# Kernel optimization log

Hardware: AMD Instinct MI355X
Metric: run time of the kernel (lower is better)

Reference implementation:

```python
import jax, jax.numpy as jnp
import numpy as np

D_MODEL = 256; D_FC = 1024; N_LEVELS = 4; N_HEADS = 8; N_POINTS = 4
D_HEAD = D_MODEL // N_HEADS
SPATIAL = np.array([[100, 100], [50, 50], [25, 25], [13, 13]], dtype=np.int64)
S_TOTAL = int((SPATIAL[:, 0] * SPATIAL[:, 1]).sum())  # 13294
BATCH = 2


def setup_inputs() -> dict:
    key = jax.random.key(0)
    ks = jax.random.split(key, 16)

    def lin(k, fi, fo):
        s = 1.0 / np.sqrt(fi)
        kw, kb = jax.random.split(k)
        W = jax.random.uniform(kw, (fi, fo), jnp.float32, -s, s)
        b = jax.random.uniform(kb, (fo,), jnp.float32, -s, s)
        return W, b

    W_off, b_off = lin(ks[0], D_MODEL, N_HEADS * N_LEVELS * N_POINTS * 2)
    W_attn, b_attn = lin(ks[1], D_MODEL, N_HEADS * N_LEVELS * N_POINTS)
    W_val, b_val = lin(ks[2], D_MODEL, D_MODEL)
    W_out, b_out = lin(ks[3], D_MODEL, D_MODEL)
    W1, b1 = lin(ks[4], D_MODEL, D_FC)
    W2, b2 = lin(ks[5], D_FC, D_MODEL)
    src = jax.random.normal(ks[6], (BATCH, S_TOTAL, D_MODEL), jnp.float32)
    pos = jax.random.normal(ks[7], (BATCH, S_TOTAL, D_MODEL), jnp.float32)
    reference_points = jax.random.uniform(ks[8], (BATCH, S_TOTAL, N_LEVELS, 2), jnp.float32)
    level_start_index = np.concatenate([[0], np.cumsum(SPATIAL[:, 0] * SPATIAL[:, 1])[:-1]]).astype(np.int64)
    return dict(src=src, pos=pos, reference_points=reference_points,
                spatial_shapes=SPATIAL, level_start_index=level_start_index,
                W_off=W_off, b_off=b_off, W_attn=W_attn, b_attn=b_attn,
                W_val=W_val, b_val=b_val, W_out=W_out, b_out=b_out,
                ln1_g=jnp.ones(D_MODEL, jnp.float32), ln1_b=jnp.zeros(D_MODEL, jnp.float32),
                W1=W1, b1=b1, W2=W2, b2=b2,
                ln2_g=jnp.ones(D_MODEL, jnp.float32), ln2_b=jnp.zeros(D_MODEL, jnp.float32))


def layernorm(x, g, b, eps=1e-5):
    mu = x.mean(-1, keepdims=True)
    var = ((x - mu) ** 2).mean(-1, keepdims=True)
    return (x - mu) * jax.lax.rsqrt(var + eps) * g + b


def ms_deform_attn(query, value_in, ref_pts, shapes,
                   W_off, b_off, W_attn, b_attn, W_val, b_val, W_out, b_out):
    N, Lq, _ = query.shape
    value = (value_in @ W_val + b_val).reshape(N, -1, N_HEADS, D_HEAD)
    off = (query @ W_off + b_off).reshape(N, Lq, N_HEADS, N_LEVELS, N_POINTS, 2)
    attn = (query @ W_attn + b_attn).reshape(N, Lq, N_HEADS, N_LEVELS * N_POINTS)
    attn = jax.nn.softmax(attn, -1).reshape(N, Lq, N_HEADS, N_LEVELS, N_POINTS)
    # offset normalizer is (W_l, H_l) per level
    norm = jnp.array([[w, h] for (h, w) in shapes], dtype=query.dtype)
    loc = ref_pts[:, :, None, :, None, :] + off / norm[None, None, None, :, None, :]
    out = jnp.zeros((N, Lq, N_HEADS, D_HEAD), query.dtype)
    start = 0
    for l, (H_, W_) in enumerate(shapes):
        v = value[:, start:start + H_ * W_].transpose(0, 2, 1, 3)  # [N, heads, HW, d]
        start += H_ * W_
        loc_l = loc[:, :, :, l]  # [N, Lq, heads, P, 2]
        # grid_sample(align_corners=False, padding_mode='zeros'): pixel = loc*size - 0.5
        px = loc_l[..., 0] * W_ - 0.5
        py = loc_l[..., 1] * H_ - 0.5
        x0 = jnp.floor(px); y0 = jnp.floor(py)
        wx = (px - x0)[..., None]; wy = (py - y0)[..., None]
        x0i = x0.astype(jnp.int32); y0i = y0.astype(jnp.int32)

        def samp(xi, yi):
            valid = (xi >= 0) & (xi < W_) & (yi >= 0) & (yi < H_)
            idx = jnp.clip(yi, 0, H_ - 1) * W_ + jnp.clip(xi, 0, W_ - 1)  # [N,Lq,heads,P]
            idx = idx.transpose(0, 2, 1, 3).reshape(N, N_HEADS, Lq * N_POINTS, 1)
            g = jnp.take_along_axis(v, idx, axis=2)  # [N,heads,Lq*P,d]
            g = g.reshape(N, N_HEADS, Lq, N_POINTS, D_HEAD).transpose(0, 2, 1, 3, 4)
            return g * valid[..., None]

        val = (samp(x0i, y0i) * (1 - wx) * (1 - wy)
               + samp(x0i + 1, y0i) * wx * (1 - wy)
               + samp(x0i, y0i + 1) * (1 - wx) * wy
               + samp(x0i + 1, y0i + 1) * wx * wy)  # [N,Lq,heads,P,d]
        out = out + (val * attn[:, :, :, l, :, None]).sum(3)
    return out.reshape(N, Lq, D_MODEL) @ W_out + b_out


def reference(src, pos, reference_points, spatial_shapes, level_start_index,
              W_off, b_off, W_attn, b_attn, W_val, b_val, W_out, b_out,
              ln1_g, ln1_b, W1, b1, W2, b2, ln2_g, ln2_b):
    shapes = [(int(spatial_shapes[l, 0]), int(spatial_shapes[l, 1])) for l in range(N_LEVELS)]
    q = src + pos
    attn_out = ms_deform_attn(q, src, reference_points, shapes,
                              W_off, b_off, W_attn, b_attn, W_val, b_val, W_out, b_out)
    x = layernorm(src + attn_out, ln1_g, ln1_b)  # dropout is identity in eval
    ffn = jax.nn.relu(x @ W1 + b1) @ W2 + b2
    return layernorm(x + ffn, ln2_g, ln2_b)
```

## Files before the change

kernel.cpp:

```cpp
#include <hip/hip_runtime.h>
#include <hip/hip_bf16.h>

#define DM 256
#define STOT 13294
#define MTOT (2 * STOT)

using bf16 = __hip_bfloat16;
typedef __attribute__((ext_vector_type(8))) short short8;
typedef __attribute__((ext_vector_type(4))) float floatx4;

#define GLDS16(g, l) __builtin_amdgcn_global_load_lds( \
    (const __attribute__((address_space(1))) void*)(g), \
    (__attribute__((address_space(3))) void*)(l), 16, 0, 0)

__device__ __forceinline__ float bu2f(unsigned u) { return __uint_as_float(u << 16); }
__device__ __forceinline__ float ldf(const float* p, size_t i) { return p[i]; }
__device__ __forceinline__ float ldf(const bf16* p, size_t i) { return __bfloat162float(p[i]); }
__device__ __forceinline__ void stf(float* p, size_t i, float v) { p[i] = v; }
__device__ __forceinline__ void stf(bf16* p, size_t i, float v) { p[i] = __float2bfloat16(v); }
__device__ __forceinline__ unsigned short f2bu(float f) {
    union { bf16 h; unsigned short u; } c; c.h = __float2bfloat16(f); return c.u;
}

__global__ void detect_dtype(const unsigned* g1, int* flag) {
    if (threadIdx.x == 0 && blockIdx.x == 0)
        *flag = (g1[0] == 0x3F800000u) ? 1 : 0;
}

struct PW { const void* W[6]; const void* B[6]; };

__global__ void prep_weights(PW a, bf16* __restrict__ WT, float* __restrict__ bf,
                             const int* __restrict__ flag) {
    const long id = (long)blockIdx.x * 256 + threadIdx.x;
    const bool f32in = (*flag != 0);
    const int sz[6]  = {65536, 65536, 32768, 65536, 262144, 262144};
    const int Ns[6]  = {256, 256, 128, 256, 1024, 256};
    const int Ksh[6] = {8, 8, 8, 8, 8, 10};
    if (id < 753664) {
        long e = id; int j = 0;
        while (e >= sz[j]) { e -= sz[j]; ++j; }
        const int n = (int)(e >> Ksh[j]);
        const int k = (int)(e & ((1 << Ksh[j]) - 1));
        const size_t src = (size_t)k * Ns[j] + n;
        float v = f32in ? ((const float*)a.W[j])[src] : __bfloat162float(((const bf16*)a.W[j])[src]);
        WT[id] = __float2bfloat16(v);
    } else if (id < 753664 + 2176) {
        long e = id - 753664; int j = 0;
        const int bsz[6] = {256, 256, 128, 256, 1024, 256};
        while (e >= bsz[j]) { e -= bsz[j]; ++j; }
        float v = f32in ? ((const float*)a.B[j])[e] : __bfloat162float(((const bf16*)a.B[j])[e]);
        bf[id - 753664] = v;
    }
}

__global__ void prep_act(const void* __restrict__ src, const void* __restrict__ pos,
                         bf16* __restrict__ sbf, bf16* __restrict__ qbf,
                         const int* __restrict__ flag) {
    const long i = ((long)blockIdx.x * 256 + threadIdx.x) * 8;
    if (i >= (long)MTOT * DM) return;
    unsigned short ps[8], pq[8];
    if (*flag) {
        const float* s = (const float*)src + i;
        const float* p = (const float*)pos + i;
        float4 a0 = *(const float4*)s, a1 = *(const float4*)(s + 4);
        float4 b0 = *(const float4*)p, b1 = *(const float4*)(p + 4);
        const float av[8] = {a0.x, a0.y, a0.z, a0.w, a1.x, a1.y, a1.z, a1.w};
        const float bv[8] = {b0.x, b0.y, b0.z, b0.w, b1.x, b1.y, b1.z, b1.w};
#pragma unroll
        for (int j = 0; j < 8; ++j) { ps[j] = f2bu(av[j]); pq[j] = f2bu(av[j] + bv[j]); }
    } else {
        const unsigned short* s = (const unsigned short*)src + i;
        const unsigned short* p = (const unsigned short*)pos + i;
        uint4 a = *(const uint4*)s, b = *(const uint4*)p;
        const unsigned* ua = (const unsigned*)&a;
        const unsigned* ub = (const unsigned*)&b;
#pragma unroll
        for (int j = 0; j < 4; ++j) {
            float a0 = bu2f(ua[j] & 0xffffu), a1 = bu2f(ua[j] >> 16);
            float b0 = bu2f(ub[j] & 0xffffu), b1 = bu2f(ub[j] >> 16);
            ps[j * 2] = f2bu(a0); ps[j * 2 + 1] = f2bu(a1);
            pq[j * 2] = f2bu(a0 + b0); pq[j * 2 + 1] = f2bu(a1 + b1);
        }
    }
    *(uint4*)((unsigned short*)sbf + i) = *(const uint4*)ps;
    *(uint4*)((unsigned short*)qbf + i) = *(const uint4*)pq;
}

template<bool RELU>
__global__ __launch_bounds__(256, 4)
void gemm_bf16(const bf16* __restrict__ A0, const bf16* __restrict__ A1, int n_a0,
               const bf16* __restrict__ WT, const float* __restrict__ bias,
               bf16* __restrict__ C0, bf16* __restrict__ C1, bf16* __restrict__ C2,
               int M, int N, int K, int ldc0) {
    __shared__ __align__(16) bf16 sh[16384];
    const int t = threadIdx.x;
    const int wave = t >> 6, lane = t & 63;
    const int bm = blockIdx.y * 128, bn = blockIdx.x * 128;
    const bf16* __restrict__ A = (bn < n_a0) ? A0 : A1;
    const int wm = (wave >> 1) * 64, wn = (wave & 1) * 64;
    const int l15 = lane & 15, quad = lane >> 4;
    const int srow = lane >> 2, sko = (lane & 3) * 8;

    floatx4 acc[4][4];
#pragma unroll
    for (int i = 0; i < 4; ++i)
#pragma unroll
        for (int j = 0; j < 4; ++j) acc[i][j] = (floatx4)0.f;

    const int nb = K >> 5;
#pragma unroll
    for (int rh = 0; rh < 2; ++rh) {
        const int rbase = rh * 64 + wave * 16;
        const int gm = min(bm + rbase + srow, M - 1);
        GLDS16(A + (size_t)gm * K + sko, &sh[rbase * 32]);
        GLDS16(WT + (size_t)(bn + rbase + srow) * K + sko, &sh[8192 + rbase * 32]);
    }
    for (int i = 0; i < nb; ++i) {
        __syncthreads();
        if (i + 1 < nb) {
            const int k0 = (i + 1) << 5;
            const int bo = ((i + 1) & 1) * 4096;
#pragma unroll
            for (int rh = 0; rh < 2; ++rh) {
                const int rbase = rh * 64 + wave * 16;
                const int gm = min(bm + rbase + srow, M - 1);
                GLDS16(A + (size_t)gm * K + k0 + sko, &sh[bo + rbase * 32]);
                GLDS16(WT + (size_t)(bn + rbase + srow) * K + k0 + sko, &sh[8192 + bo + rbase * 32]);
            }
        }
        const int bo = (i & 1) * 4096;
        short8 af[4], bfr[4];
#pragma unroll
        for (int mi = 0; mi < 4; ++mi)
            af[mi] = *(const short8*)&sh[bo + (wm + mi * 16 + l15) * 32 + quad * 8];
#pragma unroll
        for (int nj = 0; nj < 4; ++nj)
            bfr[nj] = *(const short8*)&sh[8192 + bo + (wn + nj * 16 + l15) * 32 + quad * 8];
#pragma unroll
        for (int mi = 0; mi < 4; ++mi)
#pragma unroll
            for (int nj = 0; nj < 4; ++nj)
                acc[mi][nj] = __builtin_amdgcn_mfma_f32_16x16x32_bf16(bfr[nj], af[mi], acc[mi][nj], 0, 0, 0);
    }

    bf16* C = C0; int coloff = bn, ldc = ldc0;
    if (C1 != nullptr && bn >= 256) {
        if (C2 != nullptr && bn >= 512) { C = C2; coloff = bn - 512; ldc = 128; }
        else                            { C = C1; coloff = bn - 256; ldc = 256; }
    }
    float4 bv4[4];
#pragma unroll
    for (int nj = 0; nj < 4; ++nj)
        bv4[nj] = *(const float4*)&bias[bn + wn + nj * 16 + quad * 4];
#pragma unroll
    for (int mi = 0; mi < 4; ++mi) {
        const int gm = bm + wm + mi * 16 + l15;
        if (gm >= M) continue;
#pragma unroll
        for (int nj = 0; nj < 4; ++nj) {
            const float bb[4] = {bv4[nj].x, bv4[nj].y, bv4[nj].z, bv4[nj].w};
            unsigned short pk[4];
#pragma unroll
            for (int r = 0; r < 4; ++r) {
                float v = acc[mi][nj][r] + bb[r];
                if (RELU) v = fmaxf(v, 0.f);
                pk[r] = f2bu(v);
            }
            *(uint2*)&C[(size_t)gm * ldc + coloff + wn + nj * 16 + quad * 4] = *(const uint2*)pk;
        }
    }
}

__global__ void softmax16(bf16* __restrict__ a, int total) {
    const int i = blockIdx.x * 256 + threadIdx.x;
    if (i >= total) return;
    unsigned short* p = (unsigned short*)(a + (size_t)i * 16);
    uint4 r0 = *(const uint4*)p, r1 = *(const uint4*)(p + 8);
    float w[16];
    const unsigned* u0 = (const unsigned*)&r0;
    const unsigned* u1 = (const unsigned*)&r1;
#pragma unroll
    for (int j = 0; j < 4; ++j) {
        w[j * 2] = bu2f(u0[j] & 0xffffu); w[j * 2 + 1] = bu2f(u0[j] >> 16);
        w[8 + j * 2] = bu2f(u1[j] & 0xffffu); w[8 + j * 2 + 1] = bu2f(u1[j] >> 16);
    }
    float mx = -1e30f;
#pragma unroll
    for (int j = 0; j < 16; ++j) mx = fmaxf(mx, w[j]);
    float s = 0.f;
#pragma unroll
    for (int j = 0; j < 16; ++j) { w[j] = __expf(w[j] - mx); s += w[j]; }
    const float inv = 1.f / s;
    unsigned short pk[16];
#pragma unroll
    for (int j = 0; j < 16; ++j) pk[j] = f2bu(w[j] * inv);
    *(uint4*)p = *(const uint4*)pk;
    *(uint4*)(p + 8) = *(const uint4*)(pk + 8);
}

__device__ __forceinline__ void corner(const bf16* __restrict__ base, int xi, int yi,
                                       int W_, int H_, float wgt, float* acc) {
    const bool valid = (xi >= 0) & (xi < W_) & (yi >= 0) & (yi < H_);
    const int xc = min(max(xi, 0), W_ - 1);
    const int yc = min(max(yi, 0), H_ - 1);
    const ushort4 v = *(const ushort4*)(base + (size_t)(yc * W_ + xc) * DM);
    const float m = valid ? wgt : 0.f;
    acc[0] += m * bu2f(v.x); acc[1] += m * bu2f(v.y);
    acc[2] += m * bu2f(v.z); acc[3] += m * bu2f(v.w);
}

__global__ void deform_sample(const bf16* __restrict__ value, const bf16* __restrict__ off,
                              const bf16* __restrict__ attw, const void* __restrict__ refp,
                              bf16* __restrict__ out, const int* __restrict__ flag) {
    const int t = threadIdx.x;
    const int q = blockIdx.x * 4 + (t >> 6);
    const int ln = t & 63;
    const int h = ln >> 3, dg = ln & 7;
    const int b = (q >= STOT) ? 1 : 0;

    float w[16];
    {
        const unsigned short* wp = (const unsigned short*)(attw + (size_t)q * 128 + h * 16);
        uint4 r0 = *(const uint4*)wp, r1 = *(const uint4*)(wp + 8);
        const unsigned* u0 = (const unsigned*)&r0;
        const unsigned* u1 = (const unsigned*)&r1;
#pragma unroll
        for (int j = 0; j < 4; ++j) {
            w[j * 2] = bu2f(u0[j] & 0xffffu); w[j * 2 + 1] = bu2f(u0[j] >> 16);
            w[8 + j * 2] = bu2f(u1[j] & 0xffffu); w[8 + j * 2 + 1] = bu2f(u1[j] >> 16);
        }
    }
    float of[32];
    {
        const unsigned short* op = (const unsigned short*)(off + (size_t)q * 256 + h * 32);
#pragma unroll
        for (int c = 0; c < 4; ++c) {
            uint4 r = *(const uint4*)(op + c * 8);
            const unsigned* u = (const unsigned*)&r;
#pragma unroll
            for (int j = 0; j < 4; ++j) {
                of[c * 8 + j * 2] = bu2f(u[j] & 0xffffu);
                of[c * 8 + j * 2 + 1] = bu2f(u[j] >> 16);
            }
        }
    }
    float rxy[8];
    if (*flag) {
        const float* rp = (const float*)refp + (size_t)q * 8;
        float4 r0 = *(const float4*)rp, r1 = *(const float4*)(rp + 4);
        rxy[0] = r0.x; rxy[1] = r0.y; rxy[2] = r0.z; rxy[3] = r0.w;
        rxy[4] = r1.x; rxy[5] = r1.y; rxy[6] = r1.z; rxy[7] = r1.w;
    } else {
        const unsigned short* rp = (const unsigned short*)refp + (size_t)q * 8;
        uint4 r = *(const uint4*)rp;
        const unsigned* u = (const unsigned*)&r;
#pragma unroll
        for (int j = 0; j < 4; ++j) {
            rxy[j * 2] = bu2f(u[j] & 0xffffu); rxy[j * 2 + 1] = bu2f(u[j] >> 16);
        }
    }

    const int Hs[4] = {100, 50, 25, 13};
    const int Ls[4] = {0, 10000, 12500, 13125};
    const bf16* vb = value + (size_t)(b * STOT) * DM + h * 32 + dg * 4;

    float acc[4] = {0.f, 0.f, 0.f, 0.f};
#pragma unroll
    for (int l = 0; l < 4; ++l) {
        const int W_ = Hs[l], H_ = Hs[l];
        const bf16* base = vb + (size_t)Ls[l] * DM;
        const float fw = (float)W_, fh = (float)H_;
#pragma unroll
        for (int p = 0; p < 4; ++p) {
            const float px = rxy[l * 2] * fw + of[(l * 4 + p) * 2] - 0.5f;
            const float py = rxy[l * 2 + 1] * fh + of[(l * 4 + p) * 2 + 1] - 0.5f;
            const float x0f = floorf(px), y0f = floorf(py);
            const float wx = px - x0f, wy = py - y0f;
            const int x0 = (int)x0f, y0 = (int)y0f;
            const float aw = w[l * 4 + p];
            const float ex = 1.f - wx, ey = 1.f - wy;
            corner(base, x0, y0, W_, H_, ex * ey * aw, acc);
            corner(base, x0 + 1, y0, W_, H_, wx * ey * aw, acc);
            corner(base, x0, y0 + 1, W_, H_, ex * wy * aw, acc);
            corner(base, x0 + 1, y0 + 1, W_, H_, wx * wy * aw, acc);
        }
    }
    unsigned short pk[4] = {f2bu(acc[0]), f2bu(acc[1]), f2bu(acc[2]), f2bu(acc[3])};
    *(ushort4*)((unsigned short*)out + (size_t)q * 256 + h * 32 + dg * 4) = *(const ushort4*)pk;
}

template<typename TA, typename TB, typename TW, typename TO>
__device__ __forceinline__ void add_ln_body(const TA* __restrict__ A, const TB* __restrict__ Bv,
                                            const TW* __restrict__ g, const TW* __restrict__ be,
                                            TO* __restrict__ out, float* red) {
    const int r = blockIdx.x;
    const int t = threadIdx.x;
    const size_t idx = (size_t)r * DM + t;
    float v = ldf(A, idx) + ldf(Bv, idx);
    float s = v;
#pragma unroll
    for (int o = 32; o > 0; o >>= 1) s += __shfl_down(s, o, 64);
    const int wave = t >> 6, lane = t & 63;
    if (lane == 0) red[wave] = s;
    __syncthreads();
    const float mean = (red[0] + red[1] + red[2] + red[3]) * (1.f / 256.f);
    const float c = v - mean;
    float s2 = c * c;
#pragma unroll
    for (int o = 32; o > 0; o >>= 1) s2 += __shfl_down(s2, o, 64);
    if (lane == 0) red[4 + wave] = s2;
    __syncthreads();
    const float var = (red[4] + red[5] + red[6] + red[7]) * (1.f / 256.f);
    const float y = c * rsqrtf(var + 1e-5f) * ldf(g, (size_t)t) + ldf(be, (size_t)t);
    stf(out, idx, y);
}

__global__ void add_ln1(const bf16* A, const bf16* Bv, const void* g, const void* be,
                        bf16* out, const int* flag) {
    __shared__ float red[8];
    if (*flag) add_ln_body<bf16, bf16, float, bf16>(A, Bv, (const float*)g, (const float*)be, out, red);
    else       add_ln_body<bf16, bf16, bf16, bf16>(A, Bv, (const bf16*)g, (const bf16*)be, out, red);
}

__global__ void add_ln2(const bf16* A, const bf16* Bv, const void* g, const void* be,
                        void* out, const int* flag) {
    __shared__ float red[8];
    if (*flag) add_ln_body<bf16, bf16, float, float>(A, Bv, (const float*)g, (const float*)be, (float*)out, red);
    else       add_ln_body<bf16, bf16, bf16, bf16>(A, Bv, (const bf16*)g, (const bf16*)be, (bf16*)out, red);
}

extern "C" void kernel_launch(void* const* d_in, const int* in_sizes, int n_in,
                              void* d_out, int out_size, void* d_ws, size_t ws_size,
                              hipStream_t stream) {
    const void* src   = d_in[0];
    const void* pos   = d_in[1];
    const void* refp  = d_in[2];
    const void* W_off = d_in[5];
    const void* b_off = d_in[6];
    const void* W_att = d_in[7];
    const void* b_att = d_in[8];
    const void* W_val = d_in[9];
    const void* b_val = d_in[10];
    const void* W_out = d_in[11];
    const void* b_out = d_in[12];
    const void* ln1g  = d_in[13];
    const void* ln1b  = d_in[14];
    const void* W1    = d_in[15];
    const void* b1    = d_in[16];
    const void* W2    = d_in[17];
    const void* b2    = d_in[18];
    const void* ln2g  = d_in[19];
    const void* ln2b  = d_in[20];

    const size_t M = MTOT;
    bf16* src_bf = (bf16*)d_ws;
    bf16* q_bf   = src_bf + M * 256;
    bf16* v_val  = src_bf + M * 512;
    bf16* v_off  = src_bf + M * 768;
    bf16* v_attn = src_bf + M * 1024;
    bf16* v_samp = src_bf + M * 1152;
    bf16* v_tmp  = src_bf + M * 1408;
    bf16* v_x    = q_bf;
    bf16* v_h    = v_val;
    bf16* Y      = src_bf;
    bf16* WT     = src_bf + M * 1664;
    float* biasf = (float*)(WT + 753664);
    int* flag    = (int*)(biasf + 2176);

    dim3 blk(256);
    const int mg = (MTOT + 127) / 128;

    detect_dtype<<<1, 64, 0, stream>>>((const unsigned*)ln1g, flag);

    PW pw;
    pw.W[0] = W_val; pw.W[1] = W_off; pw.W[2] = W_att; pw.W[3] = W_out; pw.W[4] = W1; pw.W[5] = W2;
    pw.B[0] = b_val; pw.B[1] = b_off; pw.B[2] = b_att; pw.B[3] = b_out; pw.B[4] = b1; pw.B[5] = b2;
    prep_weights<<<(753664 + 2176 + 255) / 256, blk, 0, stream>>>(pw, WT, biasf, flag);
    prep_act<<<(int)((M * 256 / 8 + 255) / 256), blk, 0, stream>>>(src, pos, src_bf, q_bf, flag);

    gemm_bf16<false><<<dim3(5, mg), blk, 0, stream>>>(src_bf, q_bf, 256, WT, biasf,
                                                      v_val, v_off, v_attn, MTOT, 640, 256, 256);
    softmax16<<<(MTOT * 8 + 255) / 256, blk, 0, stream>>>(v_attn, MTOT * 8);
    deform_sample<<<MTOT / 4, blk, 0, stream>>>(v_val, v_off, v_attn, refp, v_samp, flag);
    gemm_bf16<false><<<dim3(2, mg), blk, 0, stream>>>(v_samp, v_samp, 256, WT + 163840, biasf + 640,
                                                      v_tmp, nullptr, nullptr, MTOT, 256, 256, 256);
    add_ln1<<<MTOT, blk, 0, stream>>>(src_bf, v_tmp, ln1g, ln1b, v_x, flag);
    gemm_bf16<true><<<dim3(8, mg), blk, 0, stream>>>(v_x, v_x, 1024, WT + 229376, biasf + 896,
                                                     v_h, nullptr, nullptr, MTOT, 1024, 256, 1024);
    gemm_bf16<false><<<dim3(2, mg), blk, 0, stream>>>(v_h, v_h, 256, WT + 491520, biasf + 1920,
                                                      Y, nullptr, nullptr, MTOT, 256, 1024, 256);
    add_ln2<<<MTOT, blk, 0, stream>>>(v_x, Y, ln2g, ln2b, d_out, flag);
}
```

Measured before the change: 346.8 us.

## Fuse output projection with LN1, and FFN with LN2, into single kernels

Replaces the output-projection GEMM plus the separate add+layernorm kernel with one kernel that computes full 256-wide rows and applies residual, bias and LN1 in registers. It also fuses FFN1, ReLU, FFN2, residual and LN2 into one kernel, keeping the 1024-wide hidden activation in LDS chunk by chunk instead of writing it to global memory. LN parameters are converted to fp32 in the weight-prep pass. This removes several kernel launches and large intermediate round trips, at the cost of only about 208 blocks of 512 threads with one block per SM, so occupancy and parallelism are low.

```diff
diff --git a/kernel.cpp b/kernel.cpp
--- a/kernel.cpp
+++ b/kernel.cpp
@@ -14,10 +14,6 @@
     (__attribute__((address_space(3))) void*)(l), 16, 0, 0)
 
 __device__ __forceinline__ float bu2f(unsigned u) { return __uint_as_float(u << 16); }
-__device__ __forceinline__ float ldf(const float* p, size_t i) { return p[i]; }
-__device__ __forceinline__ float ldf(const bf16* p, size_t i) { return __bfloat162float(p[i]); }
-__device__ __forceinline__ void stf(float* p, size_t i, float v) { p[i] = v; }
-__device__ __forceinline__ void stf(bf16* p, size_t i, float v) { p[i] = __float2bfloat16(v); }
 __device__ __forceinline__ unsigned short f2bu(float f) {
     union { bf16 h; unsigned short u; } c; c.h = __float2bfloat16(f); return c.u;
 }
@@ -27,7 +23,7 @@
         *flag = (g1[0] == 0x3F800000u) ? 1 : 0;
 }
 
-struct PW { const void* W[6]; const void* B[6]; };
+struct PW { const void* W[6]; const void* B[10]; };
 
 __global__ void prep_weights(PW a, bf16* __restrict__ WT, float* __restrict__ bf,
                              const int* __restrict__ flag) {
@@ -44,9 +40,9 @@
         const size_t src = (size_t)k * Ns[j] + n;
         float v = f32in ? ((const float*)a.W[j])[src] : __bfloat162float(((const bf16*)a.W[j])[src]);
         WT[id] = __float2bfloat16(v);
-    } else if (id < 753664 + 2176) {
+    } else if (id < 753664 + 3200) {
         long e = id - 753664; int j = 0;
-        const int bsz[6] = {256, 256, 128, 256, 1024, 256};
+        const int bsz[10] = {256, 256, 128, 256, 1024, 256, 256, 256, 256, 256};
         while (e >= bsz[j]) { e -= bsz[j]; ++j; }
         float v = f32in ? ((const float*)a.B[j])[e] : __bfloat162float(((const bf16*)a.B[j])[e]);
         bf[id - 753664] = v;
@@ -260,14 +256,14 @@
         }
     }
 
-    const int Hs[4] = {100, 50, 25, 13};
+    const int Hs4[4] = {100, 50, 25, 13};
     const int Ls[4] = {0, 10000, 12500, 13125};
     const bf16* vb = value + (size_t)(b * STOT) * DM + h * 32 + dg * 4;
 
     float acc[4] = {0.f, 0.f, 0.f, 0.f};
 #pragma unroll
     for (int l = 0; l < 4; ++l) {
-        const int W_ = Hs[l], H_ = Hs[l];
+        const int W_ = Hs4[l], H_ = Hs4[l];
         const bf16* base = vb + (size_t)Ls[l] * DM;
         const float fw = (float)W_, fh = (float)H_;
 #pragma unroll
@@ -289,44 +285,202 @@
     *(ushort4*)((unsigned short*)out + (size_t)q * 256 + h * 32 + dg * 4) = *(const ushort4*)pk;
 }
 
-template<typename TA, typename TB, typename TW, typename TO>
-__device__ __forceinline__ void add_ln_body(const TA* __restrict__ A, const TB* __restrict__ Bv,
-                                            const TW* __restrict__ g, const TW* __restrict__ be,
-                                            TO* __restrict__ out, float* red) {
-    const int r = blockIdx.x;
-    const int t = threadIdx.x;
-    const size_t idx = (size_t)r * DM + t;
-    float v = ldf(A, idx) + ldf(Bv, idx);
-    float s = v;
-#pragma unroll
-    for (int o = 32; o > 0; o >>= 1) s += __shfl_down(s, o, 64);
-    const int wave = t >> 6, lane = t & 63;
-    if (lane == 0) red[wave] = s;
-    __syncthreads();
-    const float mean = (red[0] + red[1] + red[2] + red[3]) * (1.f / 256.f);
-    const float c = v - mean;
-    float s2 = c * c;
-#pragma unroll
-    for (int o = 32; o > 0; o >>= 1) s2 += __shfl_down(s2, o, 64);
-    if (lane == 0) red[4 + wave] = s2;
-    __syncthreads();
-    const float var = (red[4] + red[5] + red[6] + red[7]) * (1.f / 256.f);
-    const float y = c * rsqrtf(var + 1e-5f) * ldf(g, (size_t)t) + ldf(be, (size_t)t);
-    stf(out, idx, y);
-}
-
-__global__ void add_ln1(const bf16* A, const bf16* Bv, const void* g, const void* be,
-                        bf16* out, const int* flag) {
-    __shared__ float red[8];
-    if (*flag) add_ln_body<bf16, bf16, float, bf16>(A, Bv, (const float*)g, (const float*)be, out, red);
-    else       add_ln_body<bf16, bf16, bf16, bf16>(A, Bv, (const bf16*)g, (const bf16*)be, out, red);
-}
-
-__global__ void add_ln2(const bf16* A, const bf16* Bv, const void* g, const void* be,
-                        void* out, const int* flag) {
-    __shared__ float red[8];
-    if (*flag) add_ln_body<bf16, bf16, float, float>(A, Bv, (const float*)g, (const float*)be, (float*)out, red);
-    else       add_ln_body<bf16, bf16, bf16, bf16>(A, Bv, (const bf16*)g, (const bf16*)be, (bf16*)out, red);
+__global__ __launch_bounds__(512, 1)
+void out_ln1(const bf16* __restrict__ vsamp, const bf16* __restrict__ srcbf,
+             const bf16* __restrict__ WoT, const float* __restrict__ bo_f,
+             const float* __restrict__ g1, const float* __restrict__ be1,
+             bf16* __restrict__ vx, int M) {
+    __shared__ __align__(16) bf16 Bs[8 * 4096];
+    const int t = threadIdx.x, wave = t >> 6, lane = t & 63;
+    const int l15 = lane & 15, quad = lane >> 4;
+    const int srow = lane >> 2, sko = (lane & 3) * 8;
+    const int bm = blockIdx.x * 128;
+    const int mrow = bm + wave * 16 + l15;
+    const int mc = min(mrow, M - 1);
+
+    short8 af[8];
+#pragma unroll
+    for (int kk = 0; kk < 8; ++kk)
+        af[kk] = *(const short8*)(vsamp + (size_t)mc * 256 + kk * 32 + quad * 8);
+
+    floatx4 acc[16];
+#pragma unroll
+    for (int i = 0; i < 16; ++i) acc[i] = (floatx4)0.f;
+
+    for (int nc = 0; nc < 2; ++nc) {
+        __syncthreads();
+#pragma unroll
+        for (int rr = 0; rr < 8; ++rr)
+            GLDS16(WoT + (size_t)(nc * 128 + rr * 16 + srow) * 256 + wave * 32 + sko,
+                   &Bs[wave * 4096 + rr * 512]);
+        __syncthreads();
+#pragma unroll
+        for (int kk = 0; kk < 8; ++kk)
+#pragma unroll
+            for (int nj = 0; nj < 8; ++nj) {
+                short8 bfr = *(const short8*)&Bs[kk * 4096 + (nj * 16 + l15) * 32 + quad * 8];
+                acc[nc * 8 + nj] = __builtin_amdgcn_mfma_f32_16x16x32_bf16(bfr, af[kk], acc[nc * 8 + nj], 0, 0, 0);
+            }
+    }
+
+    float s = 0.f;
+#pragma unroll
+    for (int nj = 0; nj < 16; ++nj) {
+        const int n = nj * 16 + quad * 4;
+        const float4 bo = *(const float4*)&bo_f[n];
+        const uint2 ru = *(const uint2*)(srcbf + (size_t)mc * 256 + n);
+        const float rs[4] = {bu2f(ru.x & 0xffffu), bu2f(ru.x >> 16), bu2f(ru.y & 0xffffu), bu2f(ru.y >> 16)};
+        const float bb[4] = {bo.x, bo.y, bo.z, bo.w};
+#pragma unroll
+        for (int r = 0; r < 4; ++r) { acc[nj][r] += bb[r] + rs[r]; s += acc[nj][r]; }
+    }
+    s += __shfl_xor(s, 16, 64); s += __shfl_xor(s, 32, 64);
+    const float mean = s * (1.f / 256.f);
+    float s2 = 0.f;
+#pragma unroll
+    for (int nj = 0; nj < 16; ++nj)
+#pragma unroll
+        for (int r = 0; r < 4; ++r) { const float c = acc[nj][r] - mean; s2 += c * c; }
+    s2 += __shfl_xor(s2, 16, 64); s2 += __shfl_xor(s2, 32, 64);
+    const float rstd = rsqrtf(s2 * (1.f / 256.f) + 1e-5f);
+    if (mrow < M) {
+#pragma unroll
+        for (int nj = 0; nj < 16; ++nj) {
+            const int n = nj * 16 + quad * 4;
+            const float4 g = *(const float4*)&g1[n];
+            const float4 b = *(const float4*)&be1[n];
+            const float gg[4] = {g.x, g.y, g.z, g.w}, bb[4] = {b.x, b.y, b.z, b.w};
+            unsigned short pk[4];
+#pragma unroll
+            for (int r = 0; r < 4; ++r) pk[r] = f2bu((acc[nj][r] - mean) * rstd * gg[r] + bb[r]);
+            *(uint2*)&vx[(size_t)mrow * 256 + n] = *(const uint2*)pk;
+        }
+    }
+}
+
+__global__ __launch_bounds__(512, 1)
+void ffn_ln2(const bf16* __restrict__ vx, const bf16* __restrict__ W1T, const bf16* __restrict__ W2T,
+             const float* __restrict__ b1f, const float* __restrict__ b2f,
+             const float* __restrict__ g2, const float* __restrict__ be2,
+             void* __restrict__ outp, const int* __restrict__ flag, int M) {
+    __shared__ __align__(16) bf16 Bs1[8 * 4096];
+    __shared__ __align__(16) bf16 Bs2[4 * 4096];
+    __shared__ __align__(16) bf16 Hs[128 * 136];
+    const int t = threadIdx.x, wave = t >> 6, lane = t & 63;
+    const int l15 = lane & 15, quad = lane >> 4;
+    const int srow = lane >> 2, sko = (lane & 3) * 8;
+    const int bm = blockIdx.x * 128;
+    const int mrow = bm + wave * 16 + l15;
+    const int mc = min(mrow, M - 1);
+
+    short8 af[8];
+#pragma unroll
+    for (int kk = 0; kk < 8; ++kk)
+        af[kk] = *(const short8*)(vx + (size_t)mc * 256 + kk * 32 + quad * 8);
+
+    floatx4 acc2[16];
+#pragma unroll
+    for (int i = 0; i < 16; ++i) acc2[i] = (floatx4)0.f;
+
+    const int kp = wave >> 1, rh = wave & 1;
+
+    for (int ch = 0; ch < 8; ++ch) {
+        __syncthreads();
+#pragma unroll
+        for (int rr = 0; rr < 8; ++rr)
+            GLDS16(W1T + (size_t)(ch * 128 + rr * 16 + srow) * 256 + wave * 32 + sko,
+                   &Bs1[wave * 4096 + rr * 512]);
+#pragma unroll
+        for (int rr = 0; rr < 4; ++rr)
+            GLDS16(W2T + (size_t)(rh * 64 + rr * 16 + srow) * 1024 + ch * 128 + kp * 32 + sko,
+                   &Bs2[kp * 4096 + (rh * 64 + rr * 16) * 32]);
+        __syncthreads();
+
+        floatx4 acc1[8];
+#pragma unroll
+        for (int i = 0; i < 8; ++i) acc1[i] = (floatx4)0.f;
+#pragma unroll
+        for (int kk = 0; kk < 8; ++kk)
+#pragma unroll
+            for (int nj = 0; nj < 8; ++nj) {
+                short8 bfr = *(const short8*)&Bs1[kk * 4096 + (nj * 16 + l15) * 32 + quad * 8];
+                acc1[nj] = __builtin_amdgcn_mfma_f32_16x16x32_bf16(bfr, af[kk], acc1[nj], 0, 0, 0);
+            }
+#pragma unroll
+        for (int nj = 0; nj < 8; ++nj) {
+            const float4 bb = *(const float4*)&b1f[ch * 128 + nj * 16 + quad * 4];
+            const float bv[4] = {bb.x, bb.y, bb.z, bb.w};
+            unsigned short pk[4];
+#pragma unroll
+            for (int r = 0; r < 4; ++r) pk[r] = f2bu(fmaxf(acc1[nj][r] + bv[r], 0.f));
+            *(uint2*)&Hs[(wave * 16 + l15) * 136 + nj * 16 + quad * 4] = *(const uint2*)pk;
+        }
+        short8 ah[4];
+#pragma unroll
+        for (int kq = 0; kq < 4; ++kq)
+            ah[kq] = *(const short8*)&Hs[(wave * 16 + l15) * 136 + kq * 32 + quad * 8];
+#pragma unroll
+        for (int kq = 0; kq < 4; ++kq)
+#pragma unroll
+            for (int nj = 0; nj < 8; ++nj) {
+                short8 bfr = *(const short8*)&Bs2[kq * 4096 + (nj * 16 + l15) * 32 + quad * 8];
+                acc2[nj] = __builtin_amdgcn_mfma_f32_16x16x32_bf16(bfr, ah[kq], acc2[nj], 0, 0, 0);
+            }
+        __syncthreads();
+#pragma unroll
+        for (int rr = 0; rr < 4; ++rr)
+            GLDS16(W2T + (size_t)(128 + rh * 64 + rr * 16 + srow) * 1024 + ch * 128 + kp * 32 + sko,
+                   &Bs2[kp * 4096 + (rh * 64 + rr * 16) * 32]);
+        __syncthreads();
+#pragma unroll
+        for (int kq = 0; kq < 4; ++kq)
+#pragma unroll
+            for (int nj = 0; nj < 8; ++nj) {
+                short8 bfr = *(const short8*)&Bs2[kq * 4096 + (nj * 16 + l15) * 32 + quad * 8];
+                acc2[8 + nj] = __builtin_amdgcn_mfma_f32_16x16x32_bf16(bfr, ah[kq], acc2[8 + nj], 0, 0, 0);
+            }
+    }
+
+    float s = 0.f;
+#pragma unroll
+    for (int nj = 0; nj < 16; ++nj) {
+        const int n = nj * 16 + quad * 4;
+        const float4 bo = *(const float4*)&b2f[n];
+        const uint2 ru = *(const uint2*)(vx + (size_t)mc * 256 + n);
+        const float rs[4] = {bu2f(ru.x & 0xffffu), bu2f(ru.x >> 16), bu2f(ru.y & 0xffffu), bu2f(ru.y >> 16)};
+        const float bb[4] = {bo.x, bo.y, bo.z, bo.w};
+#pragma unroll
+        for (int r = 0; r < 4; ++r) { acc2[nj][r] += bb[r] + rs[r]; s += acc2[nj][r]; }
+    }
+    s += __shfl_xor(s, 16, 64); s += __shfl_xor(s, 32, 64);
+    const float mean = s * (1.f / 256.f);
+    float s2 = 0.f;
+#pragma unroll
+    for (int nj = 0; nj < 16; ++nj)
+#pragma unroll
+        for (int r = 0; r < 4; ++r) { const float c = acc2[nj][r] - mean; s2 += c * c; }
+    s2 += __shfl_xor(s2, 16, 64); s2 += __shfl_xor(s2, 32, 64);
+    const float rstd = rsqrtf(s2 * (1.f / 256.f) + 1e-5f);
+    if (mrow < M) {
+        const bool f32o = (*flag != 0);
+#pragma unroll
+        for (int nj = 0; nj < 16; ++nj) {
+            const int n = nj * 16 + quad * 4;
+            const float4 g = *(const float4*)&g2[n];
+            const float4 b = *(const float4*)&be2[n];
+            const float gg[4] = {g.x, g.y, g.z, g.w}, bb[4] = {b.x, b.y, b.z, b.w};
+            float y[4];
+#pragma unroll
+            for (int r = 0; r < 4; ++r) y[r] = (acc2[nj][r] - mean) * rstd * gg[r] + bb[r];
+            if (f32o) {
+                float4 o = {y[0], y[1], y[2], y[3]};
+                *(float4*)((float*)outp + (size_t)mrow * 256 + n) = o;
+            } else {
+                unsigned short pk[4] = {f2bu(y[0]), f2bu(y[1]), f2bu(y[2]), f2bu(y[3])};
+                *(uint2*)((bf16*)outp + (size_t)mrow * 256 + n) = *(const uint2*)pk;
+            }
+        }
+    }
 }
 
 extern "C" void kernel_launch(void* const* d_in, const int* in_sizes, int n_in,
@@ -359,13 +513,10 @@
     bf16* v_off  = src_bf + M * 768;
     bf16* v_attn = src_bf + M * 1024;
     bf16* v_samp = src_bf + M * 1152;
-    bf16* v_tmp  = src_bf + M * 1408;
-    bf16* v_x    = q_bf;
-    bf16* v_h    = v_val;
-    bf16* Y      = src_bf;
+    bf16* v_x    = src_bf + M * 1408;
     bf16* WT     = src_bf + M * 1664;
     float* biasf = (float*)(WT + 753664);
-    int* flag    = (int*)(biasf + 2176);
+    int* flag    = (int*)(biasf + 3200);
 
     dim3 blk(256);
     const int mg = (MTOT + 127) / 128;
@@ -375,19 +526,18 @@
     PW pw;
     pw.W[0] = W_val; pw.W[1] = W_off; pw.W[2] = W_att; pw.W[3] = W_out; pw.W[4] = W1; pw.W[5] = W2;
     pw.B[0] = b_val; pw.B[1] = b_off; pw.B[2] = b_att; pw.B[3] = b_out; pw.B[4] = b1; pw.B[5] = b2;
-    prep_weights<<<(753664 + 2176 + 255) / 256, blk, 0, stream>>>(pw, WT, biasf, flag);
+    pw.B[6] = ln1g;  pw.B[7] = ln1b;  pw.B[8] = ln2g;  pw.B[9] = ln2b;
+    prep_weights<<<(753664 + 3200 + 255) / 256, blk, 0, stream>>>(pw, WT, biasf, flag);
     prep_act<<<(int)((M * 256 / 8 + 255) / 256), blk, 0, stream>>>(src, pos, src_bf, q_bf, flag);
 
     gemm_bf16<false><<<dim3(5, mg), blk, 0, stream>>>(src_bf, q_bf, 256, WT, biasf,
                                                       v_val, v_off, v_attn, MTOT, 640, 256, 256);
     softmax16<<<(MTOT * 8 + 255) / 256, blk, 0, stream>>>(v_attn, MTOT * 8);
     deform_sample<<<MTOT / 4, blk, 0, stream>>>(v_val, v_off, v_attn, refp, v_samp, flag);
-    gemm_bf16<false><<<dim3(2, mg), blk, 0, stream>>>(v_samp, v_samp, 256, WT + 163840, biasf + 640,
-                                                      v_tmp, nullptr, nullptr, MTOT, 256, 256, 256);
-    add_ln1<<<MTOT, blk, 0, stream>>>(src_bf, v_tmp, ln1g, ln1b, v_x, flag);
-    gemm_bf16<true><<<dim3(8, mg), blk, 0, stream>>>(v_x, v_x, 1024, WT + 229376, biasf + 896,
-                                                     v_h, nullptr, nullptr, MTOT, 1024, 256, 1024);
-    gemm_bf16<false><<<dim3(2, mg), blk, 0, stream>>>(v_h, v_h, 256, WT + 491520, biasf + 1920,
-                                                      Y, nullptr, nullptr, MTOT, 256, 1024, 256);
-    add_ln2<<<MTOT, blk, 0, stream>>>(v_x, Y, ln2g, ln2b, d_out, flag);
-}
+    out_ln1<<<mg, dim3(512), 0, stream>>>(v_samp, src_bf, WT + 163840, biasf + 640,
+                                          biasf + 2176, biasf + 2432, v_x, MTOT);
+    ffn_ln2<<<mg, dim3(512), 0, stream>>>(v_x, WT + 229376, WT + 491520,
+                                          biasf + 896, biasf + 1920,
+                                          biasf + 2688, biasf + 2944,
+                                          d_out, flag, MTOT);
+}
```

New measurement: 322.0 us. -7.2%, faster.
